# Kernel optimization log

Hardware: AMD Instinct MI355X
Metric: run time of the kernel (lower is better)

The kernel has to match this reference:

```python
import jax, jax.numpy as jnp
import numpy as np

B, T, D = 1, 2048, 2048
HQ, HKV = 32, 8
DH = D // HQ          # 64
NREP = HQ // HKV      # 4


def _apply_rope(x, cos, sin):
    # x: (B, T, H, DH); cos/sin: (T, DH//2). Complex multiply on interleaved pairs:
    # (x0 + i*x1) * (c + i*s) -> (x0*c - x1*s, x0*s + x1*c)
    b, t, h, d = x.shape
    xr = x.reshape(b, t, h, d // 2, 2)
    x0, x1 = xr[..., 0], xr[..., 1]
    c = cos[:t][None, :, None, :]
    s = sin[:t][None, :, None, :]
    o0 = x0 * c - x1 * s
    o1 = x0 * s + x1 * c
    return jnp.stack([o0, o1], axis=-1).reshape(b, t, h, d)


def setup_inputs() -> dict:
    key = jax.random.key(0)
    ks = jax.random.split(key, 6)
    w = 0.02
    x = jax.random.normal(ks[0], (B, T, D), dtype=jnp.float32)
    Wq = jax.random.normal(ks[1], (HQ * DH, D), dtype=jnp.float32) * w
    Wk = jax.random.normal(ks[2], (HKV * DH, D), dtype=jnp.float32) * w
    Wv = jax.random.normal(ks[3], (HKV * DH, D), dtype=jnp.float32) * w
    Wo = jax.random.normal(ks[4], (D, HQ * DH), dtype=jnp.float32) * w
    # standard RoPE frequencies, theta = 10000
    inv_freq = 1.0 / (10000.0 ** (np.arange(0, DH, 2, dtype=np.float32) / DH))
    angles = np.arange(T, dtype=np.float32)[:, None] * inv_freq[None, :]  # (T, DH//2)
    rope_cos = jnp.asarray(np.cos(angles))
    rope_sin = jnp.asarray(np.sin(angles))
    mask = jnp.tril(jnp.ones((T, T), dtype=bool))  # causal
    return {"x": x, "Wq": Wq, "Wk": Wk, "Wv": Wv, "Wo": Wo,
            "rope_cos": rope_cos, "rope_sin": rope_sin, "mask": mask}


def reference(x, Wq, Wk, Wv, Wo, rope_cos, rope_sin, mask):
    b, t, d = x.shape
    q = (x @ Wq.T).reshape(b, t, HQ, DH)
    k = (x @ Wk.T).reshape(b, t, HKV, DH)
    v = (x @ Wv.T).reshape(b, t, HKV, DH)
    q = _apply_rope(q, rope_cos, rope_sin)
    k = _apply_rope(k, rope_cos, rope_sin)
    # GQA: head index = kv_head * NREP + rep (matches torch expand+reshape order)
    qg = q.reshape(b, t, HKV, NREP, DH)
    scale = jnp.sqrt(jnp.float32(DH))
    # scores: (B, HKV, NREP, T, S) without materializing expanded K
    scores = jnp.einsum('bthrd,bshd->bhrts', qg, k) / scale
    scores = jnp.where(mask[None, None, None, :t, :t], scores, -jnp.inf)
    attn = jax.nn.softmax(scores, axis=-1)
    out = jnp.einsum('bhrts,bshd->bthrd', attn, v)  # (B, T, HKV, NREP, DH)
    out = out.reshape(b, t, HQ * DH)
    return out @ Wo.T
```

## Files before the change

kernel.cpp:

```cpp
#include <hip/hip_runtime.h>
#include <math.h>
#include <stdint.h>

static constexpr int T   = 2048;
static constexpr int D   = 2048;
static constexpr int HQ  = 32;
static constexpr int HKV = 8;
static constexpr int DH  = 64;
static constexpr int DKV = HKV * DH;
static constexpr int NQKV = D + 2 * DKV;

typedef float f32x4 __attribute__((ext_vector_type(4)));
typedef __bf16 bf16x8 __attribute__((ext_vector_type(8)));
typedef __bf16 bf16x2 __attribute__((ext_vector_type(2)));
typedef unsigned short u16x8 __attribute__((ext_vector_type(8)));
typedef unsigned short u16x4 __attribute__((ext_vector_type(4)));

__device__ __forceinline__ unsigned short f2bf(float f) {
  union { float f; unsigned u; } v; v.f = f;
  unsigned u = v.u;
  return (unsigned short)((u + 0x7FFFu + ((u >> 16) & 1u)) >> 16);
}
__device__ __forceinline__ float bf2f(unsigned short b) {
  union { unsigned u; float f; } v; v.u = ((unsigned)b) << 16;
  return v.f;
}
__device__ __forceinline__ unsigned pk2bf(float a, float b) {
#if __has_builtin(__builtin_amdgcn_cvt_pk_bf16_f32)
  bf16x2 r = __builtin_amdgcn_cvt_pk_bf16_f32(a, b);
  return __builtin_bit_cast(unsigned, r);
#else
  return (unsigned)f2bf(a) | ((unsigned)f2bf(b) << 16);
#endif
}
__device__ __forceinline__ float fexp2(float x) {
#if __has_builtin(__builtin_amdgcn_exp2f)
  return __builtin_amdgcn_exp2f(x);
#else
  return exp2f(x);
#endif
}
__device__ __forceinline__ float frcp(float x) {
#if __has_builtin(__builtin_amdgcn_rcpf)
  return __builtin_amdgcn_rcpf(x);
#else
  return 1.0f / x;
#endif
}
__device__ __forceinline__ f32x4 mfma16(u16x8 a, u16x8 b, f32x4 c) {
  return __builtin_amdgcn_mfma_f32_16x16x32_bf16(
      __builtin_bit_cast(bf16x8, a), __builtin_bit_cast(bf16x8, b), c, 0, 0, 0);
}
__device__ __forceinline__ void gld16(const unsigned short* g, unsigned short* l) {
  __builtin_amdgcn_global_load_lds(
      (const __attribute__((address_space(1))) unsigned*)g,
      (__attribute__((address_space(3))) unsigned*)l, 16, 0, 0);
}

__global__ __launch_bounds__(256) void cvt_all(const float* __restrict__ x,
                                               const float* __restrict__ Wq,
                                               const float* __restrict__ Wk,
                                               const float* __restrict__ Wv,
                                               const float* __restrict__ Wo,
                                               unsigned short* __restrict__ xb,
                                               unsigned short* __restrict__ wqkv,
                                               unsigned short* __restrict__ wob) {
  int b = blockIdx.x;
  const float* src;
  unsigned short* dst;
  if (b < 2048)      { src = x;  dst = xb; }
  else if (b < 4096) { src = Wq; dst = wqkv;                          b -= 2048; }
  else if (b < 4608) { src = Wk; dst = wqkv + (size_t)D * D;          b -= 4096; }
  else if (b < 5120) { src = Wv; dst = wqkv + (size_t)(D + DKV) * D;  b -= 4608; }
  else               { src = Wo; dst = wob;                           b -= 5120; }
  size_t i = ((size_t)b * 256 + threadIdx.x) * 8;
  float4 a = *(const float4*)(src + i);
  float4 c = *(const float4*)(src + i + 4);
  uint4 r = {pk2bf(a.x, a.y), pk2bf(a.z, a.w), pk2bf(c.x, c.y), pk2bf(c.z, c.w)};
  *(uint4*)(dst + i) = r;
}

template <bool OUT_BF16>
__global__ __launch_bounds__(256) void gemm_bt_bf16(const unsigned short* __restrict__ A,
                                                    const unsigned short* __restrict__ Bt,
                                                    void* __restrict__ Cv,
                                                    int N, int K) {
  __shared__ alignas(16) unsigned short As[64 * 128];
  __shared__ alignas(16) unsigned short Bs[128 * 128];

  const int bn = blockIdx.x * 128, bm = blockIdx.y * 64;
  const int tid = threadIdx.x, w = tid >> 6, lane = tid & 63;
  const int c = lane & 15, quad = lane >> 4;

  const int r4 = lane >> 4, ch = lane & 15;
  const unsigned short* aRow = A + (size_t)(bm + w * 16 + r4) * K;
  const unsigned short* bRow = Bt + (size_t)(bn + w * 32 + r4) * K;
  unsigned short* AsW = As + (w * 16) * 128;
  unsigned short* BsW = Bs + (w * 32) * 128;

  f32x4 acc[4][2] = {};

  for (int k0 = 0; k0 < K; k0 += 128) {
#pragma unroll
    for (int j = 0; j < 4; j++) {
      const int sch = ch ^ ((j * 4 + r4) & 15);
      gld16(aRow + (size_t)(j * 4) * K + k0 + sch * 8, AsW + j * 4 * 128);
    }
#pragma unroll
    for (int j = 0; j < 8; j++) {
      const int sch = ch ^ ((j * 4 + r4) & 15);
      gld16(bRow + (size_t)(j * 4) * K + k0 + sch * 8, BsW + j * 4 * 128);
    }
    __syncthreads();

#pragma unroll
    for (int ks = 0; ks < 4; ks++) {
      const int slot = (ks * 4 + quad) ^ c;
      u16x8 a[4], b[2];
#pragma unroll
      for (int mi = 0; mi < 4; mi++)
        a[mi] = *(const u16x8*)&As[(mi * 16 + c) * 128 + slot * 8];
#pragma unroll
      for (int ni = 0; ni < 2; ni++)
        b[ni] = *(const u16x8*)&Bs[(w * 32 + ni * 16 + c) * 128 + slot * 8];
#pragma unroll
      for (int mi = 0; mi < 4; mi++)
#pragma unroll
        for (int ni = 0; ni < 2; ni++)
          acc[mi][ni] = mfma16(a[mi], b[ni], acc[mi][ni]);
    }
    __syncthreads();
  }

#pragma unroll
  for (int mi = 0; mi < 4; mi++)
#pragma unroll
    for (int ni = 0; ni < 2; ni++)
#pragma unroll
      for (int r = 0; r < 4; r++) {
        size_t row = (size_t)(bm + mi * 16 + quad * 4 + r);
        size_t col = (size_t)(bn + w * 32 + ni * 16 + c);
        if (OUT_BF16)
          ((unsigned short*)Cv)[row * N + col] = f2bf(acc[mi][ni][r]);
        else
          ((float*)Cv)[row * N + col] = acc[mi][ni][r];
      }
}

__global__ __launch_bounds__(256) void rope_tv(unsigned short* __restrict__ QKV,
                                               const float* __restrict__ cosb,
                                               const float* __restrict__ sinb,
                                               unsigned short* __restrict__ VT) {
  const int QP = T * HQ * (DH / 2);
  if (blockIdx.x < 10240) {
    int idx = blockIdx.x * 256 + threadIdx.x;
    unsigned short* p;
    int t, i;
    float sc;
    if (idx < QP) {
      t = idx / (HQ * DH / 2);
      int rem = idx - t * (HQ * DH / 2);
      i = rem & 31;
      p = QKV + (size_t)t * NQKV + rem * 2;
      sc = 0.125f * 1.44269504088896340736f;
    } else {
      int j = idx - QP;
      t = j / (HKV * DH / 2);
      int rem = j - t * (HKV * DH / 2);
      i = rem & 31;
      p = QKV + (size_t)t * NQKV + D + rem * 2;
      sc = 1.0f;
    }
    float x0 = bf2f(p[0]), x1 = bf2f(p[1]);
    float cs = cosb[t * 32 + i], sn = sinb[t * 32 + i];
    *(unsigned*)p = pk2bf((x0 * cs - x1 * sn) * sc, (x0 * sn + x1 * cs) * sc);
  } else {
    __shared__ unsigned short Ts[64][65];
    const int bid = blockIdx.x - 10240;
    const int tb = bid & 31, db = bid >> 5;
    const int tid = threadIdx.x;
    const int r = tid >> 2, c0 = (tid & 3) * 16;
    const unsigned short* src = QKV + (size_t)(tb * 64 + r) * NQKV + (D + DKV) + db * 64 + c0;
    *(u16x8*)&Ts[r][c0]     = *(const u16x8*)src;
    *(u16x8*)&Ts[r][c0 + 8] = *(const u16x8*)(src + 8);
    __syncthreads();
    u16x8 a, b;
#pragma unroll
    for (int j = 0; j < 8; j++) a[j] = Ts[c0 + j][r];
#pragma unroll
    for (int j = 0; j < 8; j++) b[j] = Ts[c0 + 8 + j][r];
    unsigned short* dst = VT + (size_t)(db * 64 + r) * T + tb * 64 + c0;
    *(u16x8*)dst = a;
    *(u16x8*)(dst + 8) = b;
  }
}

__global__ __launch_bounds__(256) void attn_kernel(const unsigned short* __restrict__ QKV,
                                                   const unsigned short* __restrict__ VT,
                                                   unsigned short* __restrict__ Ob) {
  const int kh = blockIdx.x;
  const int qt = (int)(gridDim.y - 1 - blockIdx.y);
  const int qbase = qt * 16;
  const int tid = threadIdx.x, w = tid >> 6, lane = tid & 63;
  const int c = lane & 15, quad = lane >> 4;
  const int h = kh * 4 + w;

  __shared__ alignas(16) unsigned short Kt[2][64 * 64];
  __shared__ alignas(16) unsigned short Vt[2][64 * 64];
  __shared__ alignas(16) unsigned short Pb[4 * 16 * 72];

  unsigned short* PbW = Pb + w * 16 * 72;

  u16x8 qf[2];
  {
    const unsigned short* qp = QKV + (size_t)(qbase + c) * NQKV + h * DH + quad * 8;
    qf[0] = *(const u16x8*)qp;
    qf[1] = *(const u16x8*)(qp + 32);
  }

  const int srow = lane >> 3;
  const int sch  = (lane & 7) ^ srow;
  const unsigned short* kgBase = QKV + D + (size_t)(w * 16 + srow) * NQKV + kh * DH + sch * 8;
  const unsigned short* vgBase = VT + (size_t)(kh * DH + w * 16 + srow) * T + sch * 8;

  f32x4 o[4] = {};
  float l = 0.f;

  const int nFull = qt >> 2;

#pragma unroll
  for (int j = 0; j < 2; j++) {
    gld16(kgBase + (size_t)(j * 8) * NQKV, &Kt[0][(w * 16 + j * 8) * 64]);
    gld16(vgBase + (size_t)(j * 8) * T, &Vt[0][(w * 16 + j * 8) * 64]);
  }

  for (int st = 0; st <= nFull; st++) {
    const int cur = st & 1;
    __syncthreads();
    if (st < nFull) {
#pragma unroll
      for (int j = 0; j < 2; j++) {
        gld16(kgBase + ((size_t)(st + 1) * 64 + (size_t)j * 8) * NQKV,
              &Kt[cur ^ 1][(w * 16 + j * 8) * 64]);
        gld16(vgBase + (size_t)(j * 8) * T + (st + 1) * 64,
              &Vt[cur ^ 1][(w * 16 + j * 8) * 64]);
      }
    }

    f32x4 sacc[4] = {};
#pragma unroll
    for (int ks = 0; ks < 2; ks++) {
#pragma unroll
      for (int ni = 0; ni < 4; ni++) {
        const int slot = (ks * 4 + quad) ^ (c & 7);
        u16x8 kf = *(const u16x8*)&Kt[cur][(ni * 16 + c) * 64 + slot * 8];
        sacc[ni] = mfma16(kf, qf[ks], sacc[ni]);
      }
    }

    if (st == nFull) {
      const int qrow = qbase + c;
#pragma unroll
      for (int ni = 0; ni < 4; ni++)
#pragma unroll
        for (int r = 0; r < 4; r++) {
          int key = st * 64 + ni * 16 + quad * 4 + r;
          if (key > qrow) sacc[ni][r] = -INFINITY;
        }
    }

#pragma unroll
    for (int ni = 0; ni < 4; ni++) {
      float p0 = fexp2(sacc[ni][0]);
      float p1 = fexp2(sacc[ni][1]);
      float p2 = fexp2(sacc[ni][2]);
      float p3 = fexp2(sacc[ni][3]);
      l += (p0 + p1) + (p2 + p3);
      uint2 pr = {pk2bf(p0, p1), pk2bf(p2, p3)};
      *(uint2*)&PbW[c * 72 + ni * 16 + quad * 4] = pr;
    }

#pragma unroll
    for (int ks = 0; ks < 2; ks++) {
      u16x8 pf = *(const u16x8*)&PbW[c * 72 + ks * 32 + quad * 8];
#pragma unroll
      for (int ni = 0; ni < 4; ni++) {
        const int slot = (ks * 4 + quad) ^ (c & 7);
        u16x8 vf = *(const u16x8*)&Vt[cur][(ni * 16 + c) * 64 + slot * 8];
        o[ni] = mfma16(pf, vf, o[ni]);
      }
    }
  }

  l += __shfl_xor(l, 16, 64);
  l += __shfl_xor(l, 32, 64);

  float lR[4];
#pragma unroll
  for (int r = 0; r < 4; r++) lR[r] = frcp(__shfl(l, quad * 4 + r, 64));
#pragma unroll
  for (int ni = 0; ni < 4; ni++)
#pragma unroll
    for (int r = 0; r < 4; r++) {
      size_t row = (size_t)(qbase + quad * 4 + r);
      size_t col = (size_t)(h * DH + ni * 16 + c);
      Ob[row * D + col] = f2bf(o[ni][r] * lR[r]);
    }
}

extern "C" void kernel_launch(void* const* d_in, const int* in_sizes, int n_in,
                              void* d_out, int out_size, void* d_ws, size_t ws_size,
                              hipStream_t stream) {
  const float* x  = (const float*)d_in[0];
  const float* Wq = (const float*)d_in[1];
  const float* Wk = (const float*)d_in[2];
  const float* Wv = (const float*)d_in[3];
  const float* Wo = (const float*)d_in[4];
  const float* rc = (const float*)d_in[5];
  const float* rs = (const float*)d_in[6];
  float* out = (float*)d_out;

  char* ws = (char*)d_ws;
  unsigned short* xb   = (unsigned short*)(ws);
  unsigned short* wqkv = (unsigned short*)(ws + (size_t)(8u  << 20));
  unsigned short* wob  = (unsigned short*)(ws + (size_t)(20u << 20));
  unsigned short* qkvb = (unsigned short*)(ws + (size_t)(28u << 20));
  unsigned short* Ab   = xb;
  unsigned short* VT   = wqkv;

  cvt_all<<<dim3(7168), 256, 0, stream>>>(x, Wq, Wk, Wv, Wo, xb, wqkv, wob);

  gemm_bt_bf16<true><<<dim3(NQKV / 128, T / 64), 256, 0, stream>>>(xb, wqkv, qkvb, NQKV, D);

  rope_tv<<<dim3(10240 + 256), 256, 0, stream>>>(qkvb, rc, rs, VT);

  attn_kernel<<<dim3(HKV, T / 16), 256, 0, stream>>>(qkvb, VT, Ab);

  gemm_bt_bf16<false><<<dim3(D / 128, T / 64), 256, 0, stream>>>(Ab, wob, out, D, D);
}
```

Before: 221.0 us.

## Load K/V fragments directly from global memory instead of LDS staging

```diff
diff --git a/kernel.cpp b/kernel.cpp
--- a/kernel.cpp
+++ b/kernel.cpp
@@ -195,20 +195,19 @@
   }
 }
 
-__global__ __launch_bounds__(256) void attn_kernel(const unsigned short* __restrict__ QKV,
-                                                   const unsigned short* __restrict__ VT,
-                                                   unsigned short* __restrict__ Ob) {
+__global__ __launch_bounds__(256, 4) void attn_kernel(const unsigned short* __restrict__ QKV,
+                                                      const unsigned short* __restrict__ VT,
+                                                      unsigned short* __restrict__ Ob) {
   const int kh = blockIdx.x;
-  const int qt = (int)(gridDim.y - 1 - blockIdx.y);
+  const int ny = (int)gridDim.y;
+  const int y = (int)blockIdx.y;
+  const int qt = (y < (ny >> 1)) ? (ny - 1 - 2 * y) : (2 * y - ny);
   const int qbase = qt * 16;
   const int tid = threadIdx.x, w = tid >> 6, lane = tid & 63;
   const int c = lane & 15, quad = lane >> 4;
   const int h = kh * 4 + w;
 
-  __shared__ alignas(16) unsigned short Kt[2][64 * 64];
-  __shared__ alignas(16) unsigned short Vt[2][64 * 64];
   __shared__ alignas(16) unsigned short Pb[4 * 16 * 72];
-
   unsigned short* PbW = Pb + w * 16 * 72;
 
   u16x8 qf[2];
@@ -218,45 +217,35 @@
     qf[1] = *(const u16x8*)(qp + 32);
   }
 
-  const int srow = lane >> 3;
-  const int sch  = (lane & 7) ^ srow;
-  const unsigned short* kgBase = QKV + D + (size_t)(w * 16 + srow) * NQKV + kh * DH + sch * 8;
-  const unsigned short* vgBase = VT + (size_t)(kh * DH + w * 16 + srow) * T + sch * 8;
+  const unsigned short* kBase = QKV + D + (size_t)c * NQKV + kh * DH + quad * 8;
+  const unsigned short* vBase = VT + (size_t)(kh * DH + c) * T + quad * 8;
 
   f32x4 o[4] = {};
   float l = 0.f;
 
   const int nFull = qt >> 2;
 
-#pragma unroll
-  for (int j = 0; j < 2; j++) {
-    gld16(kgBase + (size_t)(j * 8) * NQKV, &Kt[0][(w * 16 + j * 8) * 64]);
-    gld16(vgBase + (size_t)(j * 8) * T, &Vt[0][(w * 16 + j * 8) * 64]);
-  }
-
   for (int st = 0; st <= nFull; st++) {
-    const int cur = st & 1;
-    __syncthreads();
-    if (st < nFull) {
-#pragma unroll
-      for (int j = 0; j < 2; j++) {
-        gld16(kgBase + ((size_t)(st + 1) * 64 + (size_t)j * 8) * NQKV,
-              &Kt[cur ^ 1][(w * 16 + j * 8) * 64]);
-        gld16(vgBase + (size_t)(j * 8) * T + (st + 1) * 64,
-              &Vt[cur ^ 1][(w * 16 + j * 8) * 64]);
-      }
-    }
+    u16x8 kf[2][4];
+#pragma unroll
+    for (int ks = 0; ks < 2; ks++)
+#pragma unroll
+      for (int ni = 0; ni < 4; ni++)
+        kf[ks][ni] = *(const u16x8*)(kBase + (size_t)(st * 64 + ni * 16) * NQKV + ks * 32);
 
     f32x4 sacc[4] = {};
 #pragma unroll
-    for (int ks = 0; ks < 2; ks++) {
-#pragma unroll
-      for (int ni = 0; ni < 4; ni++) {
-        const int slot = (ks * 4 + quad) ^ (c & 7);
-        u16x8 kf = *(const u16x8*)&Kt[cur][(ni * 16 + c) * 64 + slot * 8];
-        sacc[ni] = mfma16(kf, qf[ks], sacc[ni]);
-      }
-    }
+    for (int ks = 0; ks < 2; ks++)
+#pragma unroll
+      for (int ni = 0; ni < 4; ni++)
+        sacc[ni] = mfma16(kf[ks][ni], qf[ks], sacc[ni]);
+
+    u16x8 vf[2][4];
+#pragma unroll
+    for (int ks = 0; ks < 2; ks++)
+#pragma unroll
+      for (int ni = 0; ni < 4; ni++)
+        vf[ks][ni] = *(const u16x8*)(vBase + (size_t)(ni * 16) * T + st * 64 + ks * 32);
 
     if (st == nFull) {
       const int qrow = qbase + c;
@@ -284,11 +273,8 @@
     for (int ks = 0; ks < 2; ks++) {
       u16x8 pf = *(const u16x8*)&PbW[c * 72 + ks * 32 + quad * 8];
 #pragma unroll
-      for (int ni = 0; ni < 4; ni++) {
-        const int slot = (ks * 4 + quad) ^ (c & 7);
-        u16x8 vf = *(const u16x8*)&Vt[cur][(ni * 16 + c) * 64 + slot * 8];
-        o[ni] = mfma16(pf, vf, o[ni]);
-      }
+      for (int ni = 0; ni < 4; ni++)
+        o[ni] = mfma16(pf, vf[ks][ni], o[ni]);
     }
   }
 
```

Result: slower. 296.0 us (+33.9%).

## Replace LDS P staging with bpermute, pair query tiles, raise occupancy

Applied to the files above, without the earlier changes.

```diff
diff --git a/kernel.cpp b/kernel.cpp
--- a/kernel.cpp
+++ b/kernel.cpp
@@ -15,6 +15,7 @@
 typedef __bf16 bf16x2 __attribute__((ext_vector_type(2)));
 typedef unsigned short u16x8 __attribute__((ext_vector_type(8)));
 typedef unsigned short u16x4 __attribute__((ext_vector_type(4)));
+typedef unsigned u32x4 __attribute__((ext_vector_type(4)));
 
 __device__ __forceinline__ unsigned short f2bf(float f) {
   union { float f; unsigned u; } v; v.f = f;
@@ -195,21 +196,21 @@
   }
 }
 
-__global__ __launch_bounds__(256) void attn_kernel(const unsigned short* __restrict__ QKV,
-                                                   const unsigned short* __restrict__ VT,
-                                                   unsigned short* __restrict__ Ob) {
+__global__ __launch_bounds__(256, 5) void attn_kernel(const unsigned short* __restrict__ QKV,
+                                                      const unsigned short* __restrict__ VT,
+                                                      unsigned short* __restrict__ Ob) {
   const int kh = blockIdx.x;
-  const int qt = (int)(gridDim.y - 1 - blockIdx.y);
+  const int ny = (int)gridDim.y;
+  const int y = (int)blockIdx.y;
+  const int qt = (y < (ny >> 1)) ? (ny - 1 - 2 * y) : (2 * y - ny);
   const int qbase = qt * 16;
   const int tid = threadIdx.x, w = tid >> 6, lane = tid & 63;
   const int c = lane & 15, quad = lane >> 4;
+  const int hi = quad >> 1;
   const int h = kh * 4 + w;
 
   __shared__ alignas(16) unsigned short Kt[2][64 * 64];
   __shared__ alignas(16) unsigned short Vt[2][64 * 64];
-  __shared__ alignas(16) unsigned short Pb[4 * 16 * 72];
-
-  unsigned short* PbW = Pb + w * 16 * 72;
 
   u16x8 qf[2];
   {
@@ -217,6 +218,9 @@
     qf[0] = *(const u16x8*)qp;
     qf[1] = *(const u16x8*)(qp + 32);
   }
+
+  const int s0 = (c + ((quad & 1) << 5)) << 2;
+  const int s1 = s0 + 64;
 
   const int srow = lane >> 3;
   const int sch  = (lane & 7) ^ srow;
@@ -248,6 +252,7 @@
     }
 
     f32x4 sacc[4] = {};
+    __builtin_amdgcn_s_setprio(1);
 #pragma unroll
     for (int ks = 0; ks < 2; ks++) {
 #pragma unroll
@@ -257,6 +262,7 @@
         sacc[ni] = mfma16(kf, qf[ks], sacc[ni]);
       }
     }
+    __builtin_amdgcn_s_setprio(0);
 
     if (st == nFull) {
       const int qrow = qbase + c;
@@ -269,6 +275,7 @@
         }
     }
 
+    unsigned wv[8];
 #pragma unroll
     for (int ni = 0; ni < 4; ni++) {
       float p0 = fexp2(sacc[ni][0]);
@@ -276,19 +283,30 @@
       float p2 = fexp2(sacc[ni][2]);
       float p3 = fexp2(sacc[ni][3]);
       l += (p0 + p1) + (p2 + p3);
-      uint2 pr = {pk2bf(p0, p1), pk2bf(p2, p3)};
-      *(uint2*)&PbW[c * 72 + ni * 16 + quad * 4] = pr;
+      wv[ni * 2]     = pk2bf(p0, p1);
+      wv[ni * 2 + 1] = pk2bf(p2, p3);
     }
 
 #pragma unroll
     for (int ks = 0; ks < 2; ks++) {
-      u16x8 pf = *(const u16x8*)&PbW[c * 72 + ks * 32 + quad * 8];
+      unsigned a0 = __builtin_amdgcn_ds_bpermute(s0, (int)wv[ks * 4 + 0]);
+      unsigned b0 = __builtin_amdgcn_ds_bpermute(s0, (int)wv[ks * 4 + 2]);
+      unsigned a1 = __builtin_amdgcn_ds_bpermute(s0, (int)wv[ks * 4 + 1]);
+      unsigned b1 = __builtin_amdgcn_ds_bpermute(s0, (int)wv[ks * 4 + 3]);
+      unsigned a2 = __builtin_amdgcn_ds_bpermute(s1, (int)wv[ks * 4 + 0]);
+      unsigned b2 = __builtin_amdgcn_ds_bpermute(s1, (int)wv[ks * 4 + 2]);
+      unsigned a3 = __builtin_amdgcn_ds_bpermute(s1, (int)wv[ks * 4 + 1]);
+      unsigned b3 = __builtin_amdgcn_ds_bpermute(s1, (int)wv[ks * 4 + 3]);
+      u32x4 pw = {hi ? b0 : a0, hi ? b1 : a1, hi ? b2 : a2, hi ? b3 : a3};
+      u16x8 pf = __builtin_bit_cast(u16x8, pw);
+      __builtin_amdgcn_s_setprio(1);
 #pragma unroll
       for (int ni = 0; ni < 4; ni++) {
         const int slot = (ks * 4 + quad) ^ (c & 7);
         u16x8 vf = *(const u16x8*)&Vt[cur][(ni * 16 + c) * 64 + slot * 8];
         o[ni] = mfma16(pf, vf, o[ni]);
       }
+      __builtin_amdgcn_s_setprio(0);
     }
   }
 
```

After: 222.1 us. Within noise of the previous version (+0.5%).

## Process two 16-row query tiles per attention block to reuse K/V tiles

Applied to the files above, without the earlier changes.

```diff
diff --git a/kernel.cpp b/kernel.cpp
--- a/kernel.cpp
+++ b/kernel.cpp
@@ -195,27 +195,34 @@
   }
 }
 
-__global__ __launch_bounds__(256) void attn_kernel(const unsigned short* __restrict__ QKV,
-                                                   const unsigned short* __restrict__ VT,
-                                                   unsigned short* __restrict__ Ob) {
+__global__ __launch_bounds__(256, 3) void attn_kernel(const unsigned short* __restrict__ QKV,
+                                                      const unsigned short* __restrict__ VT,
+                                                      unsigned short* __restrict__ Ob) {
   const int kh = blockIdx.x;
-  const int qt = (int)(gridDim.y - 1 - blockIdx.y);
-  const int qbase = qt * 16;
+  const int ny = (int)gridDim.y;
+  const int y = (int)blockIdx.y;
+  const int qt2 = (y < (ny >> 1)) ? (ny - 1 - 2 * y) : (2 * (y - (ny >> 1)));
+  const int qbase = qt2 * 32;
   const int tid = threadIdx.x, w = tid >> 6, lane = tid & 63;
   const int c = lane & 15, quad = lane >> 4;
   const int h = kh * 4 + w;
 
   __shared__ alignas(16) unsigned short Kt[2][64 * 64];
   __shared__ alignas(16) unsigned short Vt[2][64 * 64];
-  __shared__ alignas(16) unsigned short Pb[4 * 16 * 72];
-
-  unsigned short* PbW = Pb + w * 16 * 72;
-
-  u16x8 qf[2];
+  __shared__ alignas(16) unsigned short PbA[4 * 16 * 72];
+  __shared__ alignas(16) unsigned short PbB[4 * 16 * 72];
+
+  unsigned short* PbAW = PbA + w * 16 * 72;
+  unsigned short* PbBW = PbB + w * 16 * 72;
+
+  u16x8 qfA[2], qfB[2];
   {
     const unsigned short* qp = QKV + (size_t)(qbase + c) * NQKV + h * DH + quad * 8;
-    qf[0] = *(const u16x8*)qp;
-    qf[1] = *(const u16x8*)(qp + 32);
+    qfA[0] = *(const u16x8*)qp;
+    qfA[1] = *(const u16x8*)(qp + 32);
+    const unsigned short* qp2 = qp + (size_t)16 * NQKV;
+    qfB[0] = *(const u16x8*)qp2;
+    qfB[1] = *(const u16x8*)(qp2 + 32);
   }
 
   const int srow = lane >> 3;
@@ -223,10 +230,10 @@
   const unsigned short* kgBase = QKV + D + (size_t)(w * 16 + srow) * NQKV + kh * DH + sch * 8;
   const unsigned short* vgBase = VT + (size_t)(kh * DH + w * 16 + srow) * T + sch * 8;
 
-  f32x4 o[4] = {};
-  float l = 0.f;
-
-  const int nFull = qt >> 2;
+  f32x4 oA[4] = {}, oB[4] = {};
+  float lA = 0.f, lB = 0.f;
+
+  const int nFull = qt2 >> 1;
 
 #pragma unroll
   for (int j = 0; j < 2; j++) {
@@ -247,64 +254,78 @@
       }
     }
 
-    f32x4 sacc[4] = {};
+    f32x4 sA[4] = {}, sB[4] = {};
 #pragma unroll
     for (int ks = 0; ks < 2; ks++) {
 #pragma unroll
       for (int ni = 0; ni < 4; ni++) {
         const int slot = (ks * 4 + quad) ^ (c & 7);
         u16x8 kf = *(const u16x8*)&Kt[cur][(ni * 16 + c) * 64 + slot * 8];
-        sacc[ni] = mfma16(kf, qf[ks], sacc[ni]);
+        sA[ni] = mfma16(kf, qfA[ks], sA[ni]);
+        sB[ni] = mfma16(kf, qfB[ks], sB[ni]);
       }
     }
 
     if (st == nFull) {
-      const int qrow = qbase + c;
+      const int qrowA = qbase + c;
+      const int qrowB = qrowA + 16;
 #pragma unroll
       for (int ni = 0; ni < 4; ni++)
 #pragma unroll
         for (int r = 0; r < 4; r++) {
           int key = st * 64 + ni * 16 + quad * 4 + r;
-          if (key > qrow) sacc[ni][r] = -INFINITY;
+          if (key > qrowA) sA[ni][r] = -INFINITY;
+          if (key > qrowB) sB[ni][r] = -INFINITY;
         }
     }
 
 #pragma unroll
     for (int ni = 0; ni < 4; ni++) {
-      float p0 = fexp2(sacc[ni][0]);
-      float p1 = fexp2(sacc[ni][1]);
-      float p2 = fexp2(sacc[ni][2]);
-      float p3 = fexp2(sacc[ni][3]);
-      l += (p0 + p1) + (p2 + p3);
-      uint2 pr = {pk2bf(p0, p1), pk2bf(p2, p3)};
-      *(uint2*)&PbW[c * 72 + ni * 16 + quad * 4] = pr;
+      float a0 = fexp2(sA[ni][0]), a1 = fexp2(sA[ni][1]);
+      float a2 = fexp2(sA[ni][2]), a3 = fexp2(sA[ni][3]);
+      lA += (a0 + a1) + (a2 + a3);
+      uint2 pa = {pk2bf(a0, a1), pk2bf(a2, a3)};
+      *(uint2*)&PbAW[c * 72 + ni * 16 + quad * 4] = pa;
+      float b0 = fexp2(sB[ni][0]), b1 = fexp2(sB[ni][1]);
+      float b2 = fexp2(sB[ni][2]), b3 = fexp2(sB[ni][3]);
+      lB += (b0 + b1) + (b2 + b3);
+      uint2 pb = {pk2bf(b0, b1), pk2bf(b2, b3)};
+      *(uint2*)&PbBW[c * 72 + ni * 16 + quad * 4] = pb;
     }
 
 #pragma unroll
     for (int ks = 0; ks < 2; ks++) {
-      u16x8 pf = *(const u16x8*)&PbW[c * 72 + ks * 32 + quad * 8];
+      u16x8 pfA = *(const u16x8*)&PbAW[c * 72 + ks * 32 + quad * 8];
+      u16x8 pfB = *(const u16x8*)&PbBW[c * 72 + ks * 32 + quad * 8];
 #pragma unroll
       for (int ni = 0; ni < 4; ni++) {
         const int slot = (ks * 4 + quad) ^ (c & 7);
         u16x8 vf = *(const u16x8*)&Vt[cur][(ni * 16 + c) * 64 + slot * 8];
-        o[ni] = mfma16(pf, vf, o[ni]);
+        oA[ni] = mfma16(pfA, vf, oA[ni]);
+        oB[ni] = mfma16(pfB, vf, oB[ni]);
       }
     }
   }
 
-  l += __shfl_xor(l, 16, 64);
-  l += __shfl_xor(l, 32, 64);
-
-  float lR[4];
-#pragma unroll
-  for (int r = 0; r < 4; r++) lR[r] = frcp(__shfl(l, quad * 4 + r, 64));
+  lA += __shfl_xor(lA, 16, 64);
+  lA += __shfl_xor(lA, 32, 64);
+  lB += __shfl_xor(lB, 16, 64);
+  lB += __shfl_xor(lB, 32, 64);
+
+  float lRA[4], lRB[4];
+#pragma unroll
+  for (int r = 0; r < 4; r++) {
+    lRA[r] = frcp(__shfl(lA, quad * 4 + r, 64));
+    lRB[r] = frcp(__shfl(lB, quad * 4 + r, 64));
+  }
 #pragma unroll
   for (int ni = 0; ni < 4; ni++)
 #pragma unroll
     for (int r = 0; r < 4; r++) {
-      size_t row = (size_t)(qbase + quad * 4 + r);
-      size_t col = (size_t)(h * DH + ni * 16 + c);
-      Ob[row * D + col] = f2bf(o[ni][r] * lR[r]);
+      size_t rowA = (size_t)(qbase + quad * 4 + r);
+      size_t col  = (size_t)(h * DH + ni * 16 + c);
+      Ob[rowA * D + col] = f2bf(oA[ni][r] * lRA[r]);
+      Ob[(rowA + 16) * D + col] = f2bf(oB[ni][r] * lRB[r]);
     }
 }
 
@@ -334,7 +355,7 @@
 
   rope_tv<<<dim3(10240 + 256), 256, 0, stream>>>(qkvb, rc, rs, VT);
 
-  attn_kernel<<<dim3(HKV, T / 16), 256, 0, stream>>>(qkvb, VT, Ab);
+  attn_kernel<<<dim3(HKV, T / 32), 256, 0, stream>>>(qkvb, VT, Ab);
 
   gemm_bt_bf16<false><<<dim3(D / 128, T / 64), 256, 0, stream>>>(Ab, wob, out, D, D);
 }
```

After: 224.3 us. No clear change (+1.5%).
